# Kernel optimization log

Measured on AMD Instinct MI355X. Metric: run time of the kernel, lower is better.

The kernel has to match this reference:

```python
import jax, jax.numpy as jnp
import numpy as np

B, S, NQ, FFN, EMB = 8, 4096, 8, 2048, 512


def setup_inputs() -> dict:
    key = jax.random.key(0)
    k0, k1, k2, k3 = jax.random.split(key, 4)
    x = jax.random.normal(k0, (B, S, NQ), dtype=jnp.float32)
    theta = jax.random.normal(k1, (NQ,), dtype=jnp.float32)  # trainable RY angles
    W1 = jax.random.normal(k2, (NQ, FFN), dtype=jnp.float32) / np.float32(np.sqrt(NQ))
    b1 = jnp.zeros((FFN,), dtype=jnp.float32)
    W2 = jax.random.normal(k3, (FFN, EMB), dtype=jnp.float32) / np.float32(np.sqrt(FFN))
    b2 = jnp.zeros((EMB,), dtype=jnp.float32)
    return {"x": x, "theta": theta, "W1": W1, "b1": b1, "W2": W2, "b2": b2}


def reference(x, theta, W1, b1, W2, b2):
    # Quantum layer: per wire i, state RY(theta_i) RX(x_i) |0>; no entangling gates,
    # so the state is a product state and <PauliZ_i> = cos(x_i) * cos(theta_i) exactly.
    # This fuses the per-token / per-gate simulation loop into one batched expression.
    q = jnp.cos(x) * jnp.cos(theta)                     # [B, S, NQ]
    # Dropout is identity at eval time.
    h = jax.nn.relu(jnp.einsum("bsq,qf->bsf", q, W1) + b1)  # [B, S, FFN]
    out = jnp.einsum("bsf,fe->bse", h, W2) + b2             # [B, S, EMB]
    return out
```

## Files before the change

### kernel.cpp

```cpp
#include <hip/hip_runtime.h>

#define T_TOK 32768
#define NQ    8
#define FFN   2048
#define EMB   512
#define BM    128
#define BN    128
#define BK    32
#define NCHUNK (FFN / BK)

typedef __attribute__((ext_vector_type(8)))  short short8;
typedef __attribute__((ext_vector_type(16))) float f32x16;
typedef __attribute__((ext_vector_type(2)))  unsigned int u32x2;

__device__ __forceinline__ unsigned short f2bf(float f) {
  unsigned int u = __float_as_uint(f);
  u += 0x7fffu + ((u >> 16) & 1u);
  return (unsigned short)(u >> 16);
}

__device__ __forceinline__ unsigned pk2bf(float lo, float hi) {
#if __has_builtin(__builtin_amdgcn_cvt_pk_bf16_f32)
  typedef __attribute__((ext_vector_type(2))) __bf16 bf2;
  bf2 p = __builtin_amdgcn_cvt_pk_bf16_f32(lo, hi);
  return *(unsigned*)&p;
#else
  return (unsigned)f2bf(lo) | ((unsigned)f2bf(hi) << 16);
#endif
}

__global__ void prep_all(const float* __restrict__ W1,
                         const float* __restrict__ W2,
                         unsigned short* __restrict__ w1t,
                         unsigned short* __restrict__ w2t) {
  __shared__ float t[32][33];
  const int kb = blockIdx.x * 32;
  const int nb = blockIdx.y * 32;
  const int c = threadIdx.x & 31, r0 = threadIdx.x >> 5;
#pragma unroll
  for (int p = 0; p < 4; ++p) {
    int r = r0 + p * 8;
    t[r][c] = W2[(size_t)(kb + r) * EMB + nb + c];
  }
  __syncthreads();
#pragma unroll
  for (int p = 0; p < 4; ++p) {
    int r = r0 + p * 8;
    w2t[(size_t)(nb + r) * FFN + kb + c] = f2bf(t[c][r]);
  }
  if (blockIdx.x == 0) {
    const int base = blockIdx.y * 1024 + threadIdx.x * 4;
#pragma unroll
    for (int e = 0; e < 4; ++e) {
      int idx = base + e;
      int f = idx >> 3, i = idx & 7;
      w1t[idx] = f2bf(W1[i * FFN + f]);
    }
  }
}

__global__ __launch_bounds__(256, 4) void ffq_main(
    const float* __restrict__ x,
    const float* __restrict__ theta,
    const unsigned short* __restrict__ w1t,
    const float* __restrict__ b1,
    const unsigned short* __restrict__ w2t,
    const float* __restrict__ b2,
    float* __restrict__ out) {

  __shared__ __align__(16) unsigned short w2_lds[2][BN * BK];

  const int tid  = threadIdx.x;
  const int wave = tid >> 6;
  const int lane = tid & 63;
  const int nl   = lane & 31;
  const int hi   = lane >> 5;
  const int tok0 = blockIdx.x * BM;
  const int n0   = blockIdx.y * BN;

  float cth[8];
  {
    const float4* tp = (const float4*)theta;
    float4 t0 = tp[0], t1 = tp[1];
    cth[0] = __cosf(t0.x); cth[1] = __cosf(t0.y);
    cth[2] = __cosf(t0.z); cth[3] = __cosf(t0.w);
    cth[4] = __cosf(t1.x); cth[5] = __cosf(t1.y);
    cth[6] = __cosf(t1.z); cth[7] = __cosf(t1.w);
  }
  short8 bq;
  {
    const float4* xp =
        (const float4*)(x + (size_t)(tok0 + wave * 32 + nl) * NQ);
    float4 x0 = xp[0], x1 = xp[1];
    float q0 = __cosf(x0.x) * cth[0], q1 = __cosf(x0.y) * cth[1];
    float q2 = __cosf(x0.z) * cth[2], q3 = __cosf(x0.w) * cth[3];
    float q4 = __cosf(x1.x) * cth[4], q5 = __cosf(x1.y) * cth[5];
    float q6 = __cosf(x1.z) * cth[6], q7 = __cosf(x1.w) * cth[7];
    uint4 uu;
    uu.x = pk2bf(q0, q1); uu.y = pk2bf(q2, q3);
    uu.z = pk2bf(q4, q5); uu.w = pk2bf(q6, q7);
    if (hi) { uu.x = 0; uu.y = 0; uu.z = 0; uu.w = 0; }
    bq = *(short8*)&uu;
  }

  const int st_gc = (tid & 3) ^ ((tid >> 3) & 3);
  auto stage_w2 = [&](int kc_, int b_) {
    const int k0_ = kc_ * BK;
#pragma unroll
    for (int issue = 0; issue < 2; ++issue) {
      const int r = issue * 64 + (tid >> 2);
      __builtin_amdgcn_global_load_lds(
          (const __attribute__((address_space(1))) void*)(
              w2t + (size_t)(n0 + r) * FFN + k0_ + st_gc * 8),
          (__attribute__((address_space(3))) void*)(
              &w2_lds[b_][issue * 2048 + tid * 8]),
          16, 0, 0);
    }
  };

  const int swz = (nl >> 1) & 3;
  const unsigned short* rd0[2];
  const unsigned short* rd1[2];
#pragma unroll
  for (int b = 0; b < 2; ++b) {
    rd0[b] = &w2_lds[b][nl * 32 + ((0 + hi) ^ swz) * 8];
    rd1[b] = &w2_lds[b][nl * 32 + ((2 + hi) ^ swz) * 8];
  }

  f32x16 acc[4];
#pragma unroll
  for (int nt = 0; nt < 4; ++nt)
#pragma unroll
    for (int r = 0; r < 16; ++r) acc[nt][r] = 0.f;

  short8 afA[2], afB[2];
  auto gemm1 = [&](short8 aw, const float4* b4, short8& oA, short8& oB) {
    f32x16 c1;
#pragma unroll
    for (int r = 0; r < 16; ++r) c1[r] = b4[r >> 2][r & 3];
    c1 = __builtin_amdgcn_mfma_f32_32x32x16_bf16(aw, bq, c1, 0, 0, 0);
    unsigned Q[8];
#pragma unroll
    for (int p = 0; p < 8; ++p) {
      float lo = c1[2 * p]     > 0.f ? c1[2 * p]     : 0.f;
      float hl = c1[2 * p + 1] > 0.f ? c1[2 * p + 1] : 0.f;
      Q[p] = pk2bf(lo, hl);
    }
    u32x2 s0 = __builtin_amdgcn_permlane32_swap(Q[0], Q[2], false, false);
    u32x2 s1 = __builtin_amdgcn_permlane32_swap(Q[1], Q[3], false, false);
    u32x2 s2 = __builtin_amdgcn_permlane32_swap(Q[4], Q[6], false, false);
    u32x2 s3 = __builtin_amdgcn_permlane32_swap(Q[5], Q[7], false, false);
    uint4 uA; uA.x = s0[0]; uA.y = s1[0]; uA.z = s0[1]; uA.w = s1[1];
    uint4 uB; uB.x = s2[0]; uB.y = s3[0]; uB.z = s2[1]; uB.w = s3[1];
    oA = *(short8*)&uA;
    oB = *(short8*)&uB;
  };

  {
    short8 aw0 = *(const short8*)(w1t + (size_t)nl * NQ);
    float4 b40[4];
#pragma unroll
    for (int g2 = 0; g2 < 4; ++g2)
      b40[g2] = *(const float4*)(b1 + 8 * g2 + 4 * hi);
    stage_w2(0, 0);
    gemm1(aw0, b40, afA[0], afB[0]);
  }

#pragma unroll 2
  for (int kc = 0; kc < NCHUNK; ++kc) {
    const int b  = kc & 1;
    const int nc = (kc + 1 < NCHUNK) ? kc + 1 : NCHUNK - 1;

    asm volatile("s_waitcnt vmcnt(0)" ::: "memory");
    __builtin_amdgcn_s_barrier();
    __builtin_amdgcn_sched_barrier(0);

    short8 aw = *(const short8*)(w1t + (size_t)(nc * 32 + nl) * NQ);
    float4 b4[4];
#pragma unroll
    for (int g2 = 0; g2 < 4; ++g2)
      b4[g2] = *(const float4*)(b1 + nc * 32 + 8 * g2 + 4 * hi);

    stage_w2(nc, b ^ 1);

    __builtin_amdgcn_s_setprio(1);
    {
      short8 bf[4];
#pragma unroll
      for (int nt = 0; nt < 4; ++nt)
        bf[nt] = *(const short8*)(rd0[b] + nt * 1024);
#pragma unroll
      for (int nt = 0; nt < 4; ++nt)
        acc[nt] = __builtin_amdgcn_mfma_f32_32x32x16_bf16(
            afA[b], bf[nt], acc[nt], 0, 0, 0);
#pragma unroll
      for (int nt = 0; nt < 4; ++nt)
        bf[nt] = *(const short8*)(rd1[b] + nt * 1024);
#pragma unroll
      for (int nt = 0; nt < 4; ++nt)
        acc[nt] = __builtin_amdgcn_mfma_f32_32x32x16_bf16(
            afB[b], bf[nt], acc[nt], 0, 0, 0);
    }
    __builtin_amdgcn_s_setprio(0);

    gemm1(aw, b4, afA[b ^ 1], afB[b ^ 1]);
  }

  asm volatile("s_waitcnt vmcnt(0)" ::: "memory");

#pragma unroll
  for (int nt = 0; nt < 4; ++nt) {
    const int col = n0 + nt * 32 + nl;
    const float bv = b2[col];
    const int rbase = tok0 + wave * 32 + 4 * hi;
#pragma unroll
    for (int g2 = 0; g2 < 4; ++g2)
#pragma unroll
      for (int rr = 0; rr < 4; ++rr)
        out[(size_t)(rbase + 8 * g2 + rr) * EMB + col] =
            acc[nt][4 * g2 + rr] + bv;
  }
}

extern "C" void kernel_launch(void* const* d_in, const int* in_sizes, int n_in,
                              void* d_out, int out_size, void* d_ws, size_t ws_size,
                              hipStream_t stream) {
  const float* x     = (const float*)d_in[0];
  const float* theta = (const float*)d_in[1];
  const float* W1    = (const float*)d_in[2];
  const float* b1    = (const float*)d_in[3];
  const float* W2    = (const float*)d_in[4];
  const float* b2    = (const float*)d_in[5];
  float* out = (float*)d_out;

  unsigned short* w1t = (unsigned short*)d_ws;
  unsigned short* w2t = w1t + FFN * NQ;

  prep_all<<<dim3(FFN / 32, EMB / 32), 256, 0, stream>>>(W1, W2, w1t, w2t);

  dim3 grid(T_TOK / BM, EMB / BN);
  ffq_main<<<grid, 256, 0, stream>>>(x, theta, w1t, b1, w2t, b2, out);
}
```

Baseline: 174.7 us.

## Load W2 fragments directly from global memory instead of LDS staging

Removes the double-buffered LDS staging of W2 via global_load_lds and the per-chunk barriers, and has each wave read its W2 MFMA fragments straight from global memory, relying on L1/L2 for reuse across waves. The occupancy hint in launch_bounds drops from 4 to 3 to give the extra live fragment registers room. This removes barrier synchronisation and LDS traffic, but each of the four waves now fetches the same W2 data separately. Global load latency is no longer hidden by an explicit prefetch stage, and the lower occupancy may limit latency hiding further.

```diff
diff --git a/kernel.cpp b/kernel.cpp
--- a/kernel.cpp
+++ b/kernel.cpp
@@ -59,7 +59,7 @@
   }
 }
 
-__global__ __launch_bounds__(256, 4) void ffq_main(
+__global__ __launch_bounds__(256, 3) void ffq_main(
     const float* __restrict__ x,
     const float* __restrict__ theta,
     const unsigned short* __restrict__ w1t,
@@ -67,8 +67,6 @@
     const unsigned short* __restrict__ w2t,
     const float* __restrict__ b2,
     float* __restrict__ out) {
-
-  __shared__ __align__(16) unsigned short w2_lds[2][BN * BK];
 
   const int tid  = threadIdx.x;
   const int wave = tid >> 6;
@@ -103,29 +101,10 @@
     bq = *(short8*)&uu;
   }
 
-  const int st_gc = (tid & 3) ^ ((tid >> 3) & 3);
-  auto stage_w2 = [&](int kc_, int b_) {
-    const int k0_ = kc_ * BK;
-#pragma unroll
-    for (int issue = 0; issue < 2; ++issue) {
-      const int r = issue * 64 + (tid >> 2);
-      __builtin_amdgcn_global_load_lds(
-          (const __attribute__((address_space(1))) void*)(
-              w2t + (size_t)(n0 + r) * FFN + k0_ + st_gc * 8),
-          (__attribute__((address_space(3))) void*)(
-              &w2_lds[b_][issue * 2048 + tid * 8]),
-          16, 0, 0);
-    }
-  };
-
-  const int swz = (nl >> 1) & 3;
-  const unsigned short* rd0[2];
-  const unsigned short* rd1[2];
-#pragma unroll
-  for (int b = 0; b < 2; ++b) {
-    rd0[b] = &w2_lds[b][nl * 32 + ((0 + hi) ^ swz) * 8];
-    rd1[b] = &w2_lds[b][nl * 32 + ((2 + hi) ^ swz) * 8];
-  }
+  const unsigned short* w2p0 = w2t + (size_t)(n0 +  0 + nl) * FFN + hi * 8;
+  const unsigned short* w2p1 = w2t + (size_t)(n0 + 32 + nl) * FFN + hi * 8;
+  const unsigned short* w2p2 = w2t + (size_t)(n0 + 64 + nl) * FFN + hi * 8;
+  const unsigned short* w2p3 = w2t + (size_t)(n0 + 96 + nl) * FFN + hi * 8;
 
   f32x16 acc[4];
 #pragma unroll
@@ -133,7 +112,6 @@
 #pragma unroll
     for (int r = 0; r < 16; ++r) acc[nt][r] = 0.f;
 
-  short8 afA[2], afB[2];
   auto gemm1 = [&](short8 aw, const float4* b4, short8& oA, short8& oB) {
     f32x16 c1;
 #pragma unroll
@@ -156,57 +134,51 @@
     oB = *(short8*)&uB;
   };
 
+  short8 afA_c, afB_c, afA_n, afB_n;
   {
     short8 aw0 = *(const short8*)(w1t + (size_t)nl * NQ);
     float4 b40[4];
 #pragma unroll
-    for (int g2 = 0; g2 < 4; ++g2)
-      b40[g2] = *(const float4*)(b1 + 8 * g2 + 4 * hi);
-    stage_w2(0, 0);
-    gemm1(aw0, b40, afA[0], afB[0]);
+    for (int g = 0; g < 4; ++g)
+      b40[g] = *(const float4*)(b1 + 8 * g + 4 * hi);
+    gemm1(aw0, b40, afA_c, afB_c);
   }
 
 #pragma unroll 2
   for (int kc = 0; kc < NCHUNK; ++kc) {
-    const int b  = kc & 1;
     const int nc = (kc + 1 < NCHUNK) ? kc + 1 : NCHUNK - 1;
-
-    asm volatile("s_waitcnt vmcnt(0)" ::: "memory");
-    __builtin_amdgcn_s_barrier();
-    __builtin_amdgcn_sched_barrier(0);
-
-    short8 aw = *(const short8*)(w1t + (size_t)(nc * 32 + nl) * NQ);
-    float4 b4[4];
-#pragma unroll
-    for (int g2 = 0; g2 < 4; ++g2)
-      b4[g2] = *(const float4*)(b1 + nc * 32 + 8 * g2 + 4 * hi);
-
-    stage_w2(nc, b ^ 1);
-
-    __builtin_amdgcn_s_setprio(1);
+    const int ko = kc * BK;
+
+    short8 bf00 = *(const short8*)(w2p0 + ko);
+    short8 bf10 = *(const short8*)(w2p1 + ko);
+    short8 bf20 = *(const short8*)(w2p2 + ko);
+    short8 bf30 = *(const short8*)(w2p3 + ko);
+    short8 bf01 = *(const short8*)(w2p0 + ko + 16);
+    short8 bf11 = *(const short8*)(w2p1 + ko + 16);
+    short8 bf21 = *(const short8*)(w2p2 + ko + 16);
+    short8 bf31 = *(const short8*)(w2p3 + ko + 16);
+
     {
-      short8 bf[4];
-#pragma unroll
-      for (int nt = 0; nt < 4; ++nt)
-        bf[nt] = *(const short8*)(rd0[b] + nt * 1024);
-#pragma unroll
-      for (int nt = 0; nt < 4; ++nt)
-        acc[nt] = __builtin_amdgcn_mfma_f32_32x32x16_bf16(
-            afA[b], bf[nt], acc[nt], 0, 0, 0);
-#pragma unroll
-      for (int nt = 0; nt < 4; ++nt)
-        bf[nt] = *(const short8*)(rd1[b] + nt * 1024);
-#pragma unroll
-      for (int nt = 0; nt < 4; ++nt)
-        acc[nt] = __builtin_amdgcn_mfma_f32_32x32x16_bf16(
-            afB[b], bf[nt], acc[nt], 0, 0, 0);
+      short8 aw = *(const short8*)(w1t + (size_t)(nc * BK + nl) * NQ);
+      float4 b4[4];
+#pragma unroll
+      for (int g = 0; g < 4; ++g)
+        b4[g] = *(const float4*)(b1 + nc * BK + 8 * g + 4 * hi);
+      gemm1(aw, b4, afA_n, afB_n);
     }
-    __builtin_amdgcn_s_setprio(0);
-
-    gemm1(aw, b4, afA[b ^ 1], afB[b ^ 1]);
-  }
-
-  asm volatile("s_waitcnt vmcnt(0)" ::: "memory");
+
+    acc[0] = __builtin_amdgcn_mfma_f32_32x32x16_bf16(afA_c, bf00, acc[0], 0, 0, 0);
+    acc[1] = __builtin_amdgcn_mfma_f32_32x32x16_bf16(afA_c, bf10, acc[1], 0, 0, 0);
+    acc[2] = __builtin_amdgcn_mfma_f32_32x32x16_bf16(afA_c, bf20, acc[2], 0, 0, 0);
+    acc[3] = __builtin_amdgcn_mfma_f32_32x32x16_bf16(afA_c, bf30, acc[3], 0, 0, 0);
+    acc[0] = __builtin_amdgcn_mfma_f32_32x32x16_bf16(afB_c, bf01, acc[0], 0, 0, 0);
+    acc[1] = __builtin_amdgcn_mfma_f32_32x32x16_bf16(afB_c, bf11, acc[1], 0, 0, 0);
+    acc[2] = __builtin_amdgcn_mfma_f32_32x32x16_bf16(afB_c, bf21, acc[2], 0, 0, 0);
+    acc[3] = __builtin_amdgcn_mfma_f32_32x32x16_bf16(afB_c, bf31, acc[3], 0, 0, 0);
+
+    afA_c = afA_n;
+    afB_c = afB_n;
+  }
 
 #pragma unroll
   for (int nt = 0; nt < 4; ++nt) {
```

New measurement: 344.9 us. +97.4%, slower.

## Widen N tile to 256 and fold b1 into W1 via augmented K

Applied to the files above, without the earlier changes.

Doubles the output-column tile per block (BN 128→256), so each recomputed hidden fragment (the first GEMM plus ReLU) feeds eight MFMA column tiles instead of four. This halves the redundant first-layer work across the EMB dimension. It also folds bias b1 into the first MFMA by padding W1 to K=16 with a bias row and setting a constant-1 input lane, which removes the per-chunk b1 loads. Occupancy hint drops to 2 blocks/CU and accumulator registers double, and the setprio hints are removed, which risks lower latency hiding.

```diff
diff --git a/kernel.cpp b/kernel.cpp
--- a/kernel.cpp
+++ b/kernel.cpp
@@ -5,7 +5,7 @@
 #define FFN   2048
 #define EMB   512
 #define BM    128
-#define BN    128
+#define BN    256
 #define BK    32
 #define NCHUNK (FFN / BK)
 
@@ -30,13 +30,15 @@
 }
 
 __global__ void prep_all(const float* __restrict__ W1,
+                         const float* __restrict__ b1,
                          const float* __restrict__ W2,
                          unsigned short* __restrict__ w1t,
                          unsigned short* __restrict__ w2t) {
   __shared__ float t[32][33];
   const int kb = blockIdx.x * 32;
   const int nb = blockIdx.y * 32;
-  const int c = threadIdx.x & 31, r0 = threadIdx.x >> 5;
+  const int tid = threadIdx.x;
+  const int c = tid & 31, r0 = tid >> 5;
 #pragma unroll
   for (int p = 0; p < 4; ++p) {
     int r = r0 + p * 8;
@@ -49,21 +51,24 @@
     w2t[(size_t)(nb + r) * FFN + kb + c] = f2bf(t[c][r]);
   }
   if (blockIdx.x == 0) {
-    const int base = blockIdx.y * 1024 + threadIdx.x * 4;
-#pragma unroll
-    for (int e = 0; e < 4; ++e) {
-      int idx = base + e;
-      int f = idx >> 3, i = idx & 7;
-      w1t[idx] = f2bf(W1[i * FFN + f]);
-    }
-  }
-}
-
-__global__ __launch_bounds__(256, 4) void ffq_main(
+    const int f     = blockIdx.y * 128 + (tid >> 1);
+    const int khalf = tid & 1;
+    unsigned short v8[8];
+#pragma unroll
+    for (int j = 0; j < 8; ++j) {
+      const int k = khalf * 8 + j;
+      float val = (k < 8) ? W1[(size_t)k * FFN + f]
+                          : (k == 8 ? b1[f] : 0.f);
+      v8[j] = f2bf(val);
+    }
+    *(uint4*)(w1t + (size_t)f * 16 + khalf * 8) = *(uint4*)v8;
+  }
+}
+
+__global__ __launch_bounds__(256, 2) void ffq_main(
     const float* __restrict__ x,
     const float* __restrict__ theta,
     const unsigned short* __restrict__ w1t,
-    const float* __restrict__ b1,
     const unsigned short* __restrict__ w2t,
     const float* __restrict__ b2,
     float* __restrict__ out) {
@@ -99,7 +104,7 @@
     uint4 uu;
     uu.x = pk2bf(q0, q1); uu.y = pk2bf(q2, q3);
     uu.z = pk2bf(q4, q5); uu.w = pk2bf(q6, q7);
-    if (hi) { uu.x = 0; uu.y = 0; uu.z = 0; uu.w = 0; }
+    if (hi) { uu.x = 0x00003f80u; uu.y = 0; uu.z = 0; uu.w = 0; }
     bq = *(short8*)&uu;
   }
 
@@ -107,7 +112,7 @@
   auto stage_w2 = [&](int kc_, int b_) {
     const int k0_ = kc_ * BK;
 #pragma unroll
-    for (int issue = 0; issue < 2; ++issue) {
+    for (int issue = 0; issue < 4; ++issue) {
       const int r = issue * 64 + (tid >> 2);
       __builtin_amdgcn_global_load_lds(
           (const __attribute__((address_space(1))) void*)(
@@ -118,26 +123,20 @@
     }
   };
 
-  const int swz = (nl >> 1) & 3;
-  const unsigned short* rd0[2];
-  const unsigned short* rd1[2];
-#pragma unroll
-  for (int b = 0; b < 2; ++b) {
-    rd0[b] = &w2_lds[b][nl * 32 + ((0 + hi) ^ swz) * 8];
-    rd1[b] = &w2_lds[b][nl * 32 + ((2 + hi) ^ swz) * 8];
-  }
-
-  f32x16 acc[4];
-#pragma unroll
-  for (int nt = 0; nt < 4; ++nt)
+  const int swz  = (nl >> 1) & 3;
+  const int off0 = nl * 32 + ((0 + hi) ^ swz) * 8;
+  const int off1 = nl * 32 + ((2 + hi) ^ swz) * 8;
+
+  f32x16 acc[8];
+#pragma unroll
+  for (int nt = 0; nt < 8; ++nt)
 #pragma unroll
     for (int r = 0; r < 16; ++r) acc[nt][r] = 0.f;
 
-  short8 afA[2], afB[2];
-  auto gemm1 = [&](short8 aw, const float4* b4, short8& oA, short8& oB) {
+  auto gemm1 = [&](short8 aw, short8& oA, short8& oB) {
     f32x16 c1;
 #pragma unroll
-    for (int r = 0; r < 16; ++r) c1[r] = b4[r >> 2][r & 3];
+    for (int r = 0; r < 16; ++r) c1[r] = 0.f;
     c1 = __builtin_amdgcn_mfma_f32_32x32x16_bf16(aw, bq, c1, 0, 0, 0);
     unsigned Q[8];
 #pragma unroll
@@ -156,14 +155,11 @@
     oB = *(short8*)&uB;
   };
 
+  short8 afA_c, afB_c, afA_n, afB_n;
   {
-    short8 aw0 = *(const short8*)(w1t + (size_t)nl * NQ);
-    float4 b40[4];
-#pragma unroll
-    for (int g2 = 0; g2 < 4; ++g2)
-      b40[g2] = *(const float4*)(b1 + 8 * g2 + 4 * hi);
     stage_w2(0, 0);
-    gemm1(aw0, b40, afA[0], afB[0]);
+    short8 aw0 = *(const short8*)(w1t + (size_t)nl * 16 + hi * 8);
+    gemm1(aw0, afA_c, afB_c);
   }
 
 #pragma unroll 2
@@ -175,41 +171,33 @@
     __builtin_amdgcn_s_barrier();
     __builtin_amdgcn_sched_barrier(0);
 
-    short8 aw = *(const short8*)(w1t + (size_t)(nc * 32 + nl) * NQ);
-    float4 b4[4];
-#pragma unroll
-    for (int g2 = 0; g2 < 4; ++g2)
-      b4[g2] = *(const float4*)(b1 + nc * 32 + 8 * g2 + 4 * hi);
+    short8 aw = *(const short8*)(w1t + (size_t)(nc * BK + nl) * 16 + hi * 8);
 
     stage_w2(nc, b ^ 1);
 
-    __builtin_amdgcn_s_setprio(1);
-    {
-      short8 bf[4];
-#pragma unroll
-      for (int nt = 0; nt < 4; ++nt)
-        bf[nt] = *(const short8*)(rd0[b] + nt * 1024);
-#pragma unroll
-      for (int nt = 0; nt < 4; ++nt)
-        acc[nt] = __builtin_amdgcn_mfma_f32_32x32x16_bf16(
-            afA[b], bf[nt], acc[nt], 0, 0, 0);
-#pragma unroll
-      for (int nt = 0; nt < 4; ++nt)
-        bf[nt] = *(const short8*)(rd1[b] + nt * 1024);
-#pragma unroll
-      for (int nt = 0; nt < 4; ++nt)
-        acc[nt] = __builtin_amdgcn_mfma_f32_32x32x16_bf16(
-            afB[b], bf[nt], acc[nt], 0, 0, 0);
-    }
-    __builtin_amdgcn_s_setprio(0);
-
-    gemm1(aw, b4, afA[b ^ 1], afB[b ^ 1]);
+    const unsigned short* sb = &w2_lds[b][0];
+#pragma unroll
+    for (int nt = 0; nt < 8; ++nt) {
+      short8 bf = *(const short8*)(sb + off0 + nt * 1024);
+      acc[nt] = __builtin_amdgcn_mfma_f32_32x32x16_bf16(
+          afA_c, bf, acc[nt], 0, 0, 0);
+    }
+#pragma unroll
+    for (int nt = 0; nt < 8; ++nt) {
+      short8 bf = *(const short8*)(sb + off1 + nt * 1024);
+      acc[nt] = __builtin_amdgcn_mfma_f32_32x32x16_bf16(
+          afB_c, bf, acc[nt], 0, 0, 0);
+    }
+
+    gemm1(aw, afA_n, afB_n);
+    afA_c = afA_n;
+    afB_c = afB_n;
   }
 
   asm volatile("s_waitcnt vmcnt(0)" ::: "memory");
 
 #pragma unroll
-  for (int nt = 0; nt < 4; ++nt) {
+  for (int nt = 0; nt < 8; ++nt) {
     const int col = n0 + nt * 32 + nl;
     const float bv = b2[col];
     const int rbase = tok0 + wave * 32 + 4 * hi;
@@ -234,10 +222,10 @@
   float* out = (float*)d_out;
 
   unsigned short* w1t = (unsigned short*)d_ws;
-  unsigned short* w2t = w1t + FFN * NQ;
-
-  prep_all<<<dim3(FFN / 32, EMB / 32), 256, 0, stream>>>(W1, W2, w1t, w2t);
+  unsigned short* w2t = w1t + FFN * 16;
+
+  prep_all<<<dim3(FFN / 32, EMB / 32), 256, 0, stream>>>(W1, b1, W2, w1t, w2t);
 
   dim3 grid(T_TOK / BM, EMB / BN);
-  ffq_main<<<grid, 256, 0, stream>>>(x, theta, w1t, b1, w2t, b2, out);
-}
+  ffq_main<<<grid, 256, 0, stream>>>(x, theta, w1t, w2t, b2, out);
+}
```

Result: faster. 158.0 us (-9.6%).
